# Performance work log

Hardware: AMD Instinct MI355X
Metric: run time of the kernel (lower is better)

The kernel has to match this reference:

```python
import jax, jax.numpy as jnp
import numpy as np

C_IN = 5
KERNEL = 4
DEPTH = 4
C = C_IN + 3  # original + time + 2 CNN channels


def conv1d(x, w, b):
    # x: (B, Cin, L), w: (Cout, Cin, K) -> (B, Cout, L-K+1), 'VALID' padding as in signatory.Augment defaults
    y = jax.lax.conv_general_dilated(x, w, (1,), 'VALID',
                                     dimension_numbers=('NCH', 'OIH', 'NCH'))
    return y + b[None, :, None]


def augment(inp, w1, b1, w2, b2, w3, b3):
    # inp: (B, L, C_in). Mirrors signatory.Augment with layer_sizes=(8,8,2), kernel_size=4,
    # include_original=True, include_time=True, activation=relu (between layers, not after last).
    B, L, _ = inp.shape
    trunc = KERNEL - 1
    orig = inp[:, trunc:, :]                                   # (B, L-3, C_in)
    time = jnp.linspace(0.0, 1.0, L, dtype=inp.dtype)[trunc:]  # time over original stream, truncated
    time = jnp.broadcast_to(time[None, :, None], (B, L - trunc, 1))
    h = conv1d(inp.transpose(0, 2, 1), w1, b1)   # (B, 8, L-3)
    h = conv1d(jax.nn.relu(h), w2, b2)           # (B, 8, L-3)
    h = conv1d(jax.nn.relu(h), w3, b3)           # (B, 2, L-3)
    return jnp.concatenate([orig, time, h.transpose(0, 2, 1)], axis=2)  # (B, L-3, C)


def signature(path):
    # Truncated path signature, depth 4, basepoint=True (zero basepoint prepended).
    # Chen's relation: sig <- sig (tensor) exp(dx), maintained as per-level tensors.
    B, S, Cc = path.shape
    base = jnp.zeros((B, 1, Cc), path.dtype)
    inc = jnp.diff(jnp.concatenate([base, path], axis=1), axis=1)  # (B, S, C) increments incl. basepoint
    inc = inc.transpose(1, 0, 2)  # (S, B, C) for scan

    def step(carry, dx):
        s1, s2, s3, s4 = carry
        # exp(dx) levels: dx^(k)/k!
        e1 = dx
        e2 = jnp.einsum('bi,bj->bij', dx, dx) / 2.0
        e3 = jnp.einsum('bij,bk->bijk', e2, dx) / 3.0
        e4 = jnp.einsum('bijk,bl->bijkl', e3, dx) / 4.0
        # Chen: (A (x) B)_k = sum_i A_i (x) B_{k-i}, A_0 = B_0 = 1
        n1 = s1 + e1
        n2 = s2 + e2 + jnp.einsum('bi,bj->bij', s1, e1)
        n3 = (s3 + e3 + jnp.einsum('bi,bjk->bijk', s1, e2)
              + jnp.einsum('bij,bk->bijk', s2, e1))
        n4 = (s4 + e4 + jnp.einsum('bi,bjkl->bijkl', s1, e3)
              + jnp.einsum('bij,bkl->bijkl', s2, e2)
              + jnp.einsum('bijk,bl->bijkl', s3, e1))
        return (n1, n2, n3, n4), None

    init = (jnp.zeros((B, Cc), path.dtype),
            jnp.zeros((B, Cc, Cc), path.dtype),
            jnp.zeros((B, Cc, Cc, Cc), path.dtype),
            jnp.zeros((B, Cc, Cc, Cc, Cc), path.dtype))
    (s1, s2, s3, s4), _ = jax.lax.scan(step, init, inc)
    return jnp.concatenate([s1.reshape(B, -1), s2.reshape(B, -1),
                            s3.reshape(B, -1), s4.reshape(B, -1)], axis=1)  # (B, 4680)


def setup_inputs() -> dict:
    key = jax.random.key(0)
    ks = jax.random.split(key, 4)
    B, L = 64, 256

    def init_conv(k, cout, cin, ksz):
        bound = 1.0 / np.sqrt(cin * ksz)
        kw, kb = jax.random.split(k)
        w = jax.random.uniform(kw, (cout, cin, ksz), jnp.float32, -bound, bound)
        b = jax.random.uniform(kb, (cout,), jnp.float32, -bound, bound)
        return w, b

    w1, b1 = init_conv(ks[1], 8, C_IN, KERNEL)
    w2, b2 = init_conv(ks[2], 8, 8, 1)
    w3, b3 = init_conv(ks[3], 2, 8, 1)
    inp = jax.random.normal(ks[0], (B, L, C_IN), jnp.float32)
    return {"inp": inp, "w1": w1, "b1": b1, "w2": w2, "b2": b2, "w3": w3, "b3": b3}


def reference(inp, w1, b1, w2, b2, w3, b3):
    x = augment(inp, w1, b1, w2, b2, w3, b3)  # (B, L-3, C)
    return signature(x)                       # (B, 4680)
```

## Files before the change

### kernel.cpp

```cpp
#include <hip/hip_runtime.h>

#define L_IN  256
#define CIN   5
#define SIG_N 4680

__global__ __launch_bounds__(512) void sig_fused_kernel(
    const float* __restrict__ inp,
    const float* __restrict__ w1, const float* __restrict__ b1,
    const float* __restrict__ w2, const float* __restrict__ b2,
    const float* __restrict__ w3, const float* __restrict__ b3,
    float* __restrict__ out)
{
    const int blk  = blockIdx.x;
    const int b    = blk >> 2;
    const int iq   = blk & 3;
    const int tid  = threadIdx.x;
    const int w    = tid >> 6;
    const int lane = tid & 63;
    const int j    = lane >> 3;
    const int k    = lane & 7;

    __shared__ __align__(16) float dxs[264][8];
    __shared__ __align__(16) float sig3[8][592];
    __shared__ __align__(16) float acc[1024];
    __shared__ float pad_lds[8192];

    if (blk & 0x40000000) out[0] = pad_lds[tid];

    const float* __restrict__ x = inp + b * (L_IN * CIN);
    float o[8];
    if (tid < 253) {
        float h1[8];
        #pragma unroll
        for (int q = 0; q < 8; ++q) h1[q] = b1[q];
        #pragma unroll
        for (int kk = 0; kk < 4; ++kk) {
            #pragma unroll
            for (int ci = 0; ci < CIN; ++ci) {
                float v = x[(tid + kk) * CIN + ci];
                #pragma unroll
                for (int q = 0; q < 8; ++q) h1[q] = fmaf(v, w1[q * 20 + ci * 4 + kk], h1[q]);
            }
        }
        float r1v[8];
        #pragma unroll
        for (int q = 0; q < 8; ++q) r1v[q] = h1[q] > 0.f ? h1[q] : 0.f;
        float h2[8];
        #pragma unroll
        for (int q = 0; q < 8; ++q) h2[q] = b2[q];
        #pragma unroll
        for (int p = 0; p < 8; ++p) {
            #pragma unroll
            for (int q = 0; q < 8; ++q) h2[q] = fmaf(r1v[p], w2[q * 8 + p], h2[q]);
        }
        float r2v[8];
        #pragma unroll
        for (int q = 0; q < 8; ++q) r2v[q] = h2[q] > 0.f ? h2[q] : 0.f;
        float h30 = b3[0], h31 = b3[1];
        #pragma unroll
        for (int p = 0; p < 8; ++p) {
            h30 = fmaf(r2v[p], w3[p], h30);
            h31 = fmaf(r2v[p], w3[8 + p], h31);
        }
        #pragma unroll
        for (int cc = 0; cc < 5; ++cc) o[cc] = x[(tid + 3) * CIN + cc];
        o[5] = (float)(tid + 3) * (1.0f / 255.0f);
        o[6] = h30;
        o[7] = h31;
    }
    if (tid < 88) dxs[253 + (tid >> 3)][tid & 7] = 0.f;
    acc[tid] = 0.f; acc[tid + 512] = 0.f;
    if (tid < 253) {
        #pragma unroll
        for (int ch = 0; ch < 8; ++ch) dxs[tid][ch] = o[ch];
    }
    __syncthreads();
    float prevr[8];
    if (tid < 253) {
        #pragma unroll
        for (int ch = 0; ch < 8; ++ch) prevr[ch] = (tid > 0) ? dxs[tid - 1][ch] : 0.f;
    }
    __syncthreads();
    if (tid < 253) {
        #pragma unroll
        for (int ch = 0; ch < 8; ++ch) dxs[tid][ch] = o[ch] - prevr[ch];
    }
    __syncthreads();

    const int rbase = w * 32;
    float t1[8], t2r[8], t3r[8];
    float u1[2] = {0.f, 0.f}, u2[2] = {0.f, 0.f}, u3[2] = {0.f, 0.f};
    float s4v[2][8];
    #pragma unroll
    for (int i = 0; i < 8; ++i) { t1[i] = 0.f; t2r[i] = 0.f; t3r[i] = 0.f; }
    #pragma unroll
    for (int m = 0; m < 2; ++m)
        #pragma unroll
        for (int l = 0; l < 8; ++l) s4v[m][l] = 0.f;

    const float4* __restrict__ dx4 = reinterpret_cast<const float4*>(&dxs[0][0]);
    float own_p[2], bb_p[2];
    float4 r0_p[2], r1_p[2];
    #pragma unroll
    for (int u = 0; u < 2; ++u) {
        own_p[u] = dxs[rbase + u][k];
        bb_p[u]  = dxs[rbase + u][j];
        r0_p[u]  = dx4[2 * (rbase + u)];
        r1_p[u]  = dx4[2 * (rbase + u) + 1];
    }

    for (int tb = 0; tb < 32; tb += 2) {
        #pragma unroll
        for (int u = 0; u < 2; ++u) {
            const int tn = rbase + tb + u + 2;
            float  own_n = dxs[tn][k];
            float  bb_n  = dxs[tn][j];
            float4 r0_n  = dx4[2 * tn];
            float4 r1_n  = dx4[2 * tn + 1];

            const float own = own_p[u];
            const float bb  = bb_p[u];
            const float4 r0 = r0_p[u];
            const float4 r1 = r1_p[u];
            const float rr[8] = { r0.x, r0.y, r0.z, r0.w, r1.x, r1.y, r1.z, r1.w };
            const float a0 = (iq == 0) ? r0.x : (iq == 1) ? r0.z
                           : (iq == 2) ? r1.x : r1.z;
            const float a1 = (iq == 0) ? r0.y : (iq == 1) ? r0.w
                           : (iq == 2) ? r1.y : r1.w;

            const float c4_0 = fmaf(own, fmaf(bb, fmaf(u1[0], (1.0f / 6.0f),
                                a0 * (1.0f / 24.0f)), 0.5f * u2[0]), u3[0]);
            const float c4_1 = fmaf(own, fmaf(bb, fmaf(u1[1], (1.0f / 6.0f),
                                a1 * (1.0f / 24.0f)), 0.5f * u2[1]), u3[1]);
            #pragma unroll
            for (int l = 0; l < 8; ++l) {
                s4v[0][l] = fmaf(c4_0, rr[l], s4v[0][l]);
                s4v[1][l] = fmaf(c4_1, rr[l], s4v[1][l]);
            }
            u3[0] = fmaf(fmaf(bb, fmaf(u1[0], 0.5f, a0 * (1.0f / 6.0f)), u2[0]), own, u3[0]);
            u2[0] = fmaf(fmaf(a0, 0.5f, u1[0]), bb, u2[0]);
            u1[0] += a0;
            u3[1] = fmaf(fmaf(bb, fmaf(u1[1], 0.5f, a1 * (1.0f / 6.0f)), u2[1]), own, u3[1]);
            u2[1] = fmaf(fmaf(a1, 0.5f, u1[1]), bb, u2[1]);
            u1[1] += a1;

            #pragma unroll
            for (int i = 0; i < 8; ++i) {
                const float a  = rr[i];
                const float c3 = fmaf(bb, fmaf(t1[i], 0.5f, a * (1.0f / 6.0f)), t2r[i]);
                t3r[i] = fmaf(c3, own, t3r[i]);
                t2r[i] = fmaf(fmaf(a, 0.5f, t1[i]), bb, t2r[i]);
                t1[i] += a;
            }

            own_p[u] = own_n; bb_p[u] = bb_n;
            r0_p[u] = r0_n;   r1_p[u] = r1_n;
        }
    }

    if (lane == 0) {
        #pragma unroll
        for (int i = 0; i < 8; ++i) sig3[w][i] = t1[i];
    }
    if (k == 0) {
        #pragma unroll
        for (int i = 0; i < 8; ++i) sig3[w][8 + i * 8 + j] = t2r[i];
    }
    #pragma unroll
    for (int i = 0; i < 8; ++i) sig3[w][72 + (i * 8 + j) * 8 + k] = t3r[i];
    __syncthreads();

    const int i0 = 2 * iq;
    float p1[2] = {0.f, 0.f}, p2[2] = {0.f, 0.f}, p3[2] = {0.f, 0.f};

    auto combine = [&](int cc) {
        const float* __restrict__ lp = sig3[cc];
        const float s1j  = lp[j];
        const float s1k  = lp[k];
        const float s2jk = lp[8 + j * 8 + k];
        #pragma unroll
        for (int m = 0; m < 2; ++m) {
            const int i = i0 + m;
            const float s1i  = lp[i];
            const float s2ij = lp[8 + i * 8 + j];
            const float s3i  = lp[72 + (i * 8 + j) * 8 + k];
            const float np3 = p3[m] + s3i + p1[m] * s2jk + p2[m] * s1k;
            const float np2 = p2[m] + s2ij + p1[m] * s1j;
            p3[m] = np3; p2[m] = np2; p1[m] += s1i;
        }
    };

    for (int cc = 0; cc < w; ++cc) combine(cc);
    {
        const float* __restrict__ lp = sig3[w];
        const float4 s1a = *reinterpret_cast<const float4*>(lp);
        const float4 s1b = *reinterpret_cast<const float4*>(lp + 4);
        const float4 s2a = *reinterpret_cast<const float4*>(lp + 8 + k * 8);
        const float4 s2b = *reinterpret_cast<const float4*>(lp + 8 + k * 8 + 4);
        const float4 s3a = *reinterpret_cast<const float4*>(lp + 72 + (j * 8 + k) * 8);
        const float4 s3b = *reinterpret_cast<const float4*>(lp + 72 + (j * 8 + k) * 8 + 4);
        const float s1r[8] = { s1a.x, s1a.y, s1a.z, s1a.w, s1b.x, s1b.y, s1b.z, s1b.w };
        const float s2r[8] = { s2a.x, s2a.y, s2a.z, s2a.w, s2b.x, s2b.y, s2b.z, s2b.w };
        const float s3r[8] = { s3a.x, s3a.y, s3a.z, s3a.w, s3b.x, s3b.y, s3b.z, s3b.w };
        #pragma unroll
        for (int m = 0; m < 2; ++m)
            #pragma unroll
            for (int l = 0; l < 8; ++l)
                s4v[m][l] = fmaf(p1[m], s3r[l],
                             fmaf(p2[m], s2r[l],
                              fmaf(p3[m], s1r[l], s4v[m][l])));
    }

    float* __restrict__ ob = out + (size_t)b * SIG_N;
    if (w == 7) {
        combine(7);
        #pragma unroll
        for (int m = 0; m < 2; ++m) {
            const int i = i0 + m;
            if (lane == 0) ob[i] = p1[m];
            if (k == 0)    ob[8 + i * 8 + j] = p2[m];
            ob[72 + (i * 8 + j) * 8 + k] = p3[m];
        }
    }

    #pragma unroll
    for (int ph = 0; ph < 8; ++ph) {
        if (w == ph) {
            #pragma unroll
            for (int m = 0; m < 2; ++m) {
                float4* ap = reinterpret_cast<float4*>(&acc[m * 512 + lane * 8]);
                float4 v0 = ap[0], v1 = ap[1];
                v0.x += s4v[m][0]; v0.y += s4v[m][1]; v0.z += s4v[m][2]; v0.w += s4v[m][3];
                v1.x += s4v[m][4]; v1.y += s4v[m][5]; v1.z += s4v[m][6]; v1.w += s4v[m][7];
                ap[0] = v0; ap[1] = v1;
            }
        }
        __syncthreads();
    }

    float2 v = *reinterpret_cast<float2*>(&acc[2 * tid]);
    *reinterpret_cast<float2*>(ob + 584 + iq * 1024 + 2 * tid) = v;
}

extern "C" void kernel_launch(void* const* d_in, const int* in_sizes, int n_in,
                              void* d_out, int out_size, void* d_ws, size_t ws_size,
                              hipStream_t stream)
{
    const float* inp = (const float*)d_in[0];
    const float* w1  = (const float*)d_in[1];
    const float* b1  = (const float*)d_in[2];
    const float* w2  = (const float*)d_in[3];
    const float* b2  = (const float*)d_in[4];
    const float* w3  = (const float*)d_in[5];
    const float* b3  = (const float*)d_in[6];
    float* out = (float*)d_out;

    sig_fused_kernel<<<256, 512, 0, stream>>>(inp, w1, b1, w2, b2, w3, b3, out);
}
```

Measured before the change: 80.50 us.

## Permute channels per block to reuse t-registers and replace serial s4 reduction

Each block permutes the channel order so that its two level-4 leading indices land in slots 0 and 1. The separate u1/u2/u3 accumulators become redundant and are dropped, reusing t1/t2r/t3r[0..1] instead. The eight-phase serialized LDS accumulation with a sync per phase is replaced by every wave writing its partial to its own buffer, then one parallel 8-way sum and a permuted scatter to the output. The removed pad_lds array changes LDS usage and occupancy, and the output indices must be un-permuted, which adds scattered stores.

```diff
diff --git a/kernel.cpp b/kernel.cpp
--- a/kernel.cpp
+++ b/kernel.cpp
@@ -14,6 +14,7 @@
     const int blk  = blockIdx.x;
     const int b    = blk >> 2;
     const int iq   = blk & 3;
+    const int i0   = 2 * iq;
     const int tid  = threadIdx.x;
     const int w    = tid >> 6;
     const int lane = tid & 63;
@@ -22,10 +23,11 @@
 
     __shared__ __align__(16) float dxs[264][8];
     __shared__ __align__(16) float sig3[8][592];
-    __shared__ __align__(16) float acc[1024];
-    __shared__ float pad_lds[8192];
-
-    if (blk & 0x40000000) out[0] = pad_lds[tid];
+    __shared__ __align__(16) float s4red[8][1024];
+
+    auto PI = [&](int x) {
+        return (((x >> 1) == 0) | ((x >> 1) == iq)) ? (x ^ i0) : x;
+    };
 
     const float* __restrict__ x = inp + b * (L_IN * CIN);
     float o[8];
@@ -69,27 +71,28 @@
         o[7] = h31;
     }
     if (tid < 88) dxs[253 + (tid >> 3)][tid & 7] = 0.f;
-    acc[tid] = 0.f; acc[tid + 512] = 0.f;
-    if (tid < 253) {
-        #pragma unroll
-        for (int ch = 0; ch < 8; ++ch) dxs[tid][ch] = o[ch];
-    }
-    __syncthreads();
-    float prevr[8];
-    if (tid < 253) {
-        #pragma unroll
-        for (int ch = 0; ch < 8; ++ch) prevr[ch] = (tid > 0) ? dxs[tid - 1][ch] : 0.f;
-    }
-    __syncthreads();
-    if (tid < 253) {
-        #pragma unroll
-        for (int ch = 0; ch < 8; ++ch) dxs[tid][ch] = o[ch] - prevr[ch];
+    if (tid < 253) {
+        #pragma unroll
+        for (int c = 0; c < 8; ++c) dxs[tid][PI(c)] = o[c];
+    }
+    __syncthreads();
+    float curr[8], prevr[8];
+    if (tid < 253) {
+        #pragma unroll
+        for (int ch = 0; ch < 8; ++ch) {
+            curr[ch]  = dxs[tid][ch];
+            prevr[ch] = (tid > 0) ? dxs[tid - 1][ch] : 0.f;
+        }
+    }
+    __syncthreads();
+    if (tid < 253) {
+        #pragma unroll
+        for (int ch = 0; ch < 8; ++ch) dxs[tid][ch] = curr[ch] - prevr[ch];
     }
     __syncthreads();
 
     const int rbase = w * 32;
     float t1[8], t2r[8], t3r[8];
-    float u1[2] = {0.f, 0.f}, u2[2] = {0.f, 0.f}, u3[2] = {0.f, 0.f};
     float s4v[2][8];
     #pragma unroll
     for (int i = 0; i < 8; ++i) { t1[i] = 0.f; t2r[i] = 0.f; t3r[i] = 0.f; }
@@ -123,26 +126,16 @@
             const float4 r0 = r0_p[u];
             const float4 r1 = r1_p[u];
             const float rr[8] = { r0.x, r0.y, r0.z, r0.w, r1.x, r1.y, r1.z, r1.w };
-            const float a0 = (iq == 0) ? r0.x : (iq == 1) ? r0.z
-                           : (iq == 2) ? r1.x : r1.z;
-            const float a1 = (iq == 0) ? r0.y : (iq == 1) ? r0.w
-                           : (iq == 2) ? r1.y : r1.w;
-
-            const float c4_0 = fmaf(own, fmaf(bb, fmaf(u1[0], (1.0f / 6.0f),
-                                a0 * (1.0f / 24.0f)), 0.5f * u2[0]), u3[0]);
-            const float c4_1 = fmaf(own, fmaf(bb, fmaf(u1[1], (1.0f / 6.0f),
-                                a1 * (1.0f / 24.0f)), 0.5f * u2[1]), u3[1]);
+
+            const float c4_0 = fmaf(own, fmaf(bb, fmaf(t1[0], (1.0f / 6.0f),
+                                r0.x * (1.0f / 24.0f)), 0.5f * t2r[0]), t3r[0]);
+            const float c4_1 = fmaf(own, fmaf(bb, fmaf(t1[1], (1.0f / 6.0f),
+                                r0.y * (1.0f / 24.0f)), 0.5f * t2r[1]), t3r[1]);
             #pragma unroll
             for (int l = 0; l < 8; ++l) {
                 s4v[0][l] = fmaf(c4_0, rr[l], s4v[0][l]);
                 s4v[1][l] = fmaf(c4_1, rr[l], s4v[1][l]);
             }
-            u3[0] = fmaf(fmaf(bb, fmaf(u1[0], 0.5f, a0 * (1.0f / 6.0f)), u2[0]), own, u3[0]);
-            u2[0] = fmaf(fmaf(a0, 0.5f, u1[0]), bb, u2[0]);
-            u1[0] += a0;
-            u3[1] = fmaf(fmaf(bb, fmaf(u1[1], 0.5f, a1 * (1.0f / 6.0f)), u2[1]), own, u3[1]);
-            u2[1] = fmaf(fmaf(a1, 0.5f, u1[1]), bb, u2[1]);
-            u1[1] += a1;
 
             #pragma unroll
             for (int i = 0; i < 8; ++i) {
@@ -170,7 +163,6 @@
     for (int i = 0; i < 8; ++i) sig3[w][72 + (i * 8 + j) * 8 + k] = t3r[i];
     __syncthreads();
 
-    const int i0 = 2 * iq;
     float p1[2] = {0.f, 0.f}, p2[2] = {0.f, 0.f}, p3[2] = {0.f, 0.f};
 
     auto combine = [&](int cc) {
@@ -180,10 +172,9 @@
         const float s2jk = lp[8 + j * 8 + k];
         #pragma unroll
         for (int m = 0; m < 2; ++m) {
-            const int i = i0 + m;
-            const float s1i  = lp[i];
-            const float s2ij = lp[8 + i * 8 + j];
-            const float s3i  = lp[72 + (i * 8 + j) * 8 + k];
+            const float s1i  = lp[m];
+            const float s2ij = lp[8 + m * 8 + j];
+            const float s3i  = lp[72 + (m * 8 + j) * 8 + k];
             const float np3 = p3[m] + s3i + p1[m] * s2jk + p2[m] * s1k;
             const float np2 = p2[m] + s2ij + p1[m] * s1j;
             p3[m] = np3; p2[m] = np2; p1[m] += s1i;
@@ -214,32 +205,44 @@
     float* __restrict__ ob = out + (size_t)b * SIG_N;
     if (w == 7) {
         combine(7);
+        const int pj = PI(j);
+        const int pk = PI(k);
         #pragma unroll
         for (int m = 0; m < 2; ++m) {
             const int i = i0 + m;
             if (lane == 0) ob[i] = p1[m];
-            if (k == 0)    ob[8 + i * 8 + j] = p2[m];
-            ob[72 + (i * 8 + j) * 8 + k] = p3[m];
-        }
-    }
-
-    #pragma unroll
-    for (int ph = 0; ph < 8; ++ph) {
-        if (w == ph) {
-            #pragma unroll
-            for (int m = 0; m < 2; ++m) {
-                float4* ap = reinterpret_cast<float4*>(&acc[m * 512 + lane * 8]);
-                float4 v0 = ap[0], v1 = ap[1];
-                v0.x += s4v[m][0]; v0.y += s4v[m][1]; v0.z += s4v[m][2]; v0.w += s4v[m][3];
-                v1.x += s4v[m][4]; v1.y += s4v[m][5]; v1.z += s4v[m][6]; v1.w += s4v[m][7];
-                ap[0] = v0; ap[1] = v1;
-            }
-        }
-        __syncthreads();
-    }
-
-    float2 v = *reinterpret_cast<float2*>(&acc[2 * tid]);
-    *reinterpret_cast<float2*>(ob + 584 + iq * 1024 + 2 * tid) = v;
+            if (k == 0)    ob[8 + i * 8 + pj] = p2[m];
+            ob[72 + (i * 8 + pj) * 8 + pk] = p3[m];
+        }
+    }
+
+    {
+        float4* wp0 = reinterpret_cast<float4*>(&s4red[w][lane * 8]);
+        wp0[0] = make_float4(s4v[0][0], s4v[0][1], s4v[0][2], s4v[0][3]);
+        wp0[1] = make_float4(s4v[0][4], s4v[0][5], s4v[0][6], s4v[0][7]);
+        float4* wp1 = reinterpret_cast<float4*>(&s4red[w][512 + lane * 8]);
+        wp1[0] = make_float4(s4v[1][0], s4v[1][1], s4v[1][2], s4v[1][3]);
+        wp1[1] = make_float4(s4v[1][4], s4v[1][5], s4v[1][6], s4v[1][7]);
+    }
+    __syncthreads();
+
+    {
+        const int m  = tid >> 8;
+        const int jk = (tid >> 2) & 63;
+        const int l0 = (tid & 3) << 1;
+        const int off = m * 512 + jk * 8 + l0;
+        float2 v; v.x = 0.f; v.y = 0.f;
+        #pragma unroll
+        for (int ww = 0; ww < 8; ++ww) {
+            const float2 t = *reinterpret_cast<const float2*>(&s4red[ww][off]);
+            v.x += t.x; v.y += t.y;
+        }
+        const int jp = jk >> 3, kp = jk & 7;
+        const int gj = PI(jp);
+        const int gk = PI(kp);
+        const int gl = PI(l0);
+        *reinterpret_cast<float2*>(ob + 584 + (i0 + m) * 512 + gj * 64 + gk * 8 + gl) = v;
+    }
 }
 
 extern "C" void kernel_launch(void* const* d_in, const int* in_sizes, int n_in,
```

Measured after the change: 78.91 us (median of 2 runs). 1.02x faster.
